# Optimization experiments

Measured on AMD Instinct MI355X. Metric: run time of the kernel, lower is better.

Reference implementation:

```python
import jax, jax.numpy as jnp
import numpy as np

B, C, H, W = 8, 256, 64, 64


def setup_inputs() -> dict:
    key = jax.random.key(0)
    ks = jax.random.split(key, 8)
    s = 1.0 / np.sqrt(C)
    return {
        "x": jax.random.normal(ks[0], (B, C, H, W), dtype=jnp.float32),
        "Wq": jax.random.normal(ks[1], (C, C), dtype=jnp.float32) * s,
        "bq": jax.random.normal(ks[2], (C,), dtype=jnp.float32) * 0.01,
        "Wk": jax.random.normal(ks[3], (C, C), dtype=jnp.float32) * s,
        "bk": jax.random.normal(ks[4], (C,), dtype=jnp.float32) * 0.01,
        "Wv": jax.random.normal(ks[5], (C, C), dtype=jnp.float32) * s,
        "bv": jax.random.normal(ks[6], (C,), dtype=jnp.float32) * 0.01,
        "gamma": jax.random.normal(ks[7], (1,), dtype=jnp.float32) * 0.1,
    }


def reference(x, Wq, bq, Wk, bk, Wv, bv, gamma):
    b, c, h, w = x.shape
    xf = x.reshape(b, c, h * w)                       # (B, C, N)
    # 1x1 conv == per-pixel linear: out_c = W @ in_c + bias
    q = jnp.einsum('oc,bcn->bon', Wq, xf) + bq[None, :, None]
    k = jnp.einsum('oc,bcn->bon', Wk, xf) + bk[None, :, None]
    v = jnp.einsum('oc,bcn->bon', Wv, xf) + bv[None, :, None]
    # attention_map[b, i, j] = sum_c q[b, c, i] * k[b, c, j]  (no scaling in original)
    scores = jnp.einsum('bci,bcj->bij', q, k)         # (B, N, N)
    attn = jax.nn.softmax(scores, axis=-1)
    # out[b, c, i] = sum_j v[b, c, j] * attn[b, i, j]
    out = jnp.einsum('bcj,bij->bci', v, attn)
    out = out.reshape(b, c, h, w)
    return x + gamma[0] * out
```

## Files before the change

kernel.cpp:

```cpp
#include <hip/hip_runtime.h>

#define BATCH 8
#define CCH 256
#define NPOS 4096

typedef __bf16 bf16x8 __attribute__((ext_vector_type(8)));
typedef float f32x4 __attribute__((ext_vector_type(4)));
typedef int i32x4 __attribute__((ext_vector_type(4)));

typedef const __attribute__((address_space(1))) void GAS;
typedef __attribute__((address_space(3))) void LAS;

#define CFENCE() __asm__ volatile("" ::: "memory")
#define WAIT_VM8()  do { CFENCE(); __builtin_amdgcn_s_waitcnt(0x0F78); CFENCE(); } while (0)
#define WAIT_LGKM0() do { CFENCE(); __builtin_amdgcn_s_waitcnt(0xC07F); CFENCE(); } while (0)
#define BAR_RAW() do { CFENCE(); __builtin_amdgcn_s_barrier(); CFENCE(); } while (0)

__device__ __forceinline__ unsigned short f2bf(float f) {
  unsigned u = __builtin_bit_cast(unsigned, f);
  u += 0x7fffu + ((u >> 16) & 1u);
  return (unsigned short)(u >> 16);
}

__device__ __forceinline__ bf16x8 ld_bf8(const unsigned short* p) {
  i32x4 t = *reinterpret_cast<const i32x4*>(p);
  return __builtin_bit_cast(bf16x8, t);
}

__global__ void cvt_kernel(const float* __restrict__ Wq,
                           const float* __restrict__ Wk,
                           const float* __restrict__ Wv,
                           unsigned short* __restrict__ dst)
{
  const int idx = blockIdx.x * 256 + threadIdx.x;
  const float* src = (idx < 65536) ? Wq : ((idx < 131072) ? Wk : Wv);
  dst[idx] = f2bf(src[idx & 65535]);
}

__global__ __launch_bounds__(256, 3)
void qkv_kernel(const float* __restrict__ x,
                const unsigned short* __restrict__ Wall,
                const float* __restrict__ bq,
                const float* __restrict__ bk,
                const float* __restrict__ bv,
                unsigned short* __restrict__ qT,
                unsigned short* __restrict__ kT,
                unsigned short* __restrict__ vG)
{
  __shared__ __align__(16) unsigned short xT[64 * 264];
  __shared__ __align__(16) unsigned short tbuf[64 * 72];

  const int b     = blockIdx.x;
  const int i0    = blockIdx.y * 64;
  const int obase = blockIdx.z * 64;
  const int tid = threadIdx.x;
  const int w   = tid >> 6;
  const int l   = tid & 63;
  const int n   = l & 15;
  const int q4  = l >> 4;

  {
    const float* xp = x + ((size_t)b * CCH + tid) * NPOS + i0;
#pragma unroll
    for (int it = 0; it < 16; ++it) {
      f32x4 f = *reinterpret_cast<const f32x4*>(xp + it * 4);
#pragma unroll
      for (int e = 0; e < 4; ++e) xT[(it * 4 + e) * 264 + tid] = f2bf(f[e]);
    }
  }
  __syncthreads();

  const size_t qbase = (size_t)b * NPOS * CCH;

  for (int s = 0; s < 3; ++s) {
    const unsigned short* Wp = Wall + s * 65536 + (size_t)(obase + w * 16 + n) * CCH + q4 * 8;
    bf16x8 wfr[8];
#pragma unroll
    for (int kk = 0; kk < 8; ++kk) wfr[kk] = ld_bf8(Wp + kk * 32);

    const float* bias = (s == 0) ? bq : (s == 1) ? bk : bv;
    float bo[4];
#pragma unroll
    for (int r = 0; r < 4; ++r) bo[r] = bias[obase + w * 16 + q4 * 4 + r];

    f32x4 acc[4];
#pragma unroll
    for (int pt = 0; pt < 4; ++pt) {
      acc[pt] = {0.f, 0.f, 0.f, 0.f};
#pragma unroll
      for (int kk = 0; kk < 8; ++kk) {
        bf16x8 bfr = ld_bf8(&xT[(pt * 16 + n) * 264 + kk * 32 + q4 * 8]);
        acc[pt] = __builtin_amdgcn_mfma_f32_16x16x32_bf16(wfr[kk], bfr, acc[pt], 0, 0, 0);
      }
    }

    if (s) __syncthreads();
    if (s < 2) {
#pragma unroll
      for (int pt = 0; pt < 4; ++pt)
#pragma unroll
        for (int r = 0; r < 4; ++r)
          tbuf[(pt * 16 + n) * 72 + w * 16 + q4 * 4 + r] = f2bf(acc[pt][r] + bo[r]);
    } else {
#pragma unroll
      for (int pt = 0; pt < 4; ++pt)
#pragma unroll
        for (int r = 0; r < 4; ++r)
          tbuf[(w * 16 + q4 * 4 + r) * 72 + pt * 16 + n] = f2bf(acc[pt][r] + bo[r]);
    }
    __syncthreads();

    if (s < 2) {
      unsigned short* dst = (s == 0 ? qT : kT) + qbase;
#pragma unroll
      for (int it = 0; it < 2; ++it) {
        const int idx = it * 256 + tid;
        const int pos = idx >> 3, ow = (idx & 7) * 8;
        i32x4 d = *reinterpret_cast<const i32x4*>(&tbuf[pos * 72 + ow]);
        *reinterpret_cast<i32x4*>(&dst[(size_t)(i0 + pos) * CCH + obase + ow]) = d;
      }
    } else {
#pragma unroll
      for (int it = 0; it < 2; ++it) {
        const int idx = it * 256 + tid;
        const int o = idx >> 3, pw = (idx & 7) * 8;
        i32x4 d = *reinterpret_cast<const i32x4*>(&tbuf[o * 72 + pw]);
        *reinterpret_cast<i32x4*>(&vG[qbase + (size_t)(obase + o) * NPOS + i0 + pw]) = d;
      }
    }
  }
}

__global__ __launch_bounds__(256, 2)
void attn_kernel(const unsigned short* __restrict__ qT,
                 const unsigned short* __restrict__ kT,
                 const unsigned short* __restrict__ vG,
                 const float* __restrict__ x,
                 const float* __restrict__ gamma,
                 float* __restrict__ out)
{
  __shared__ __align__(16) unsigned short kbuf[2][64 * 256];
  __shared__ __align__(16) unsigned short pbuf[64 * 72];
  __shared__ float stat_lds[64];

  const int b   = blockIdx.x;
  const int i0  = blockIdx.y * 64;
  const int tid = threadIdx.x;
  const int w   = tid >> 6;
  const int l   = tid & 63;
  const int n   = l & 15;
  const int q4  = l >> 4;
  const int nsw = n & 7;

  const unsigned short* qTb = qT + (size_t)b * NPOS * CCH;
  const unsigned short* kTb = kT + (size_t)b * NPOS * CCH;
  const unsigned short* vb  = vG + (size_t)b * NPOS * CCH;

  bf16x8 afr[8];
  {
    const unsigned short* qrow = qTb + (size_t)(i0 + w * 16 + n) * CCH + q4 * 8;
#pragma unroll
    for (int kk = 0; kk < 8; ++kk)
      afr[kk] = ld_bf8(qrow + kk * 32);
  }

  {
#pragma unroll
    for (int it = 0; it < 8; ++it) {
      const int t = w * 8 + it;
      const int j = 2 * t + (l >> 5);
      const int gp = l & 31;
      const int g  = gp ^ (j & 7);
      const unsigned short* src = kTb + (size_t)j * CCH + g * 8;
      unsigned short* dst = &kbuf[0][t * 512];
      __builtin_amdgcn_global_load_lds((GAS*)src, (LAS*)dst, 16, 0, 0);
    }
  }

  f32x4 O[16];
#pragma unroll
  for (int t = 0; t < 16; ++t) O[t] = {0.f, 0.f, 0.f, 0.f};
  float mrow[4] = {-1e30f, -1e30f, -1e30f, -1e30f};
  float lrow[4] = {0.f, 0.f, 0.f, 0.f};

  for (int jt = 0; jt < 64; ++jt) {
    const int j0 = jt * 64;
    const unsigned short* kb = kbuf[jt & 1];

    i32x4 vreg[8];
#pragma unroll
    for (int ct = 0; ct < 4; ++ct) {
      const unsigned short* vp = vb + (size_t)(w * 64 + ct * 16 + n) * NPOS + j0 + q4 * 8;
      vreg[ct * 2]     = *reinterpret_cast<const i32x4*>(vp);
      vreg[ct * 2 + 1] = *reinterpret_cast<const i32x4*>(vp + 32);
    }

    WAIT_VM8();
    BAR_RAW();

    f32x4 sacc[4];
#pragma unroll
    for (int nt = 0; nt < 4; ++nt) {
      const unsigned short* krow = kb + (nt * 16 + n) * 256;
      sacc[nt] = {0.f, 0.f, 0.f, 0.f};
#pragma unroll
      for (int kk = 0; kk < 8; ++kk) {
        const int gp = (kk * 4 + q4) ^ nsw;
        bf16x8 bfr = ld_bf8(krow + gp * 8);
        sacc[nt] = __builtin_amdgcn_mfma_f32_16x16x32_bf16(afr[kk], bfr, sacc[nt], 0, 0, 0);
      }
    }

    float a_r[4];
#pragma unroll
    for (int r = 0; r < 4; ++r) {
      float tm = fmaxf(fmaxf(sacc[0][r], sacc[1][r]), fmaxf(sacc[2][r], sacc[3][r]));
      tm = fmaxf(tm, __shfl_xor(tm, 1));
      tm = fmaxf(tm, __shfl_xor(tm, 2));
      tm = fmaxf(tm, __shfl_xor(tm, 4));
      tm = fmaxf(tm, __shfl_xor(tm, 8));
      const float mnew = fmaxf(mrow[r], tm);
      a_r[r] = __expf(mrow[r] - mnew);
      float s = 0.f;
#pragma unroll
      for (int nt = 0; nt < 4; ++nt) {
        const float p = __expf(sacc[nt][r] - mnew);
        sacc[nt][r] = p;
        s += p;
      }
      s += __shfl_xor(s, 1);
      s += __shfl_xor(s, 2);
      s += __shfl_xor(s, 4);
      s += __shfl_xor(s, 8);
      lrow[r] = lrow[r] * a_r[r] + s;
      mrow[r] = mnew;
    }

    if (n == 0) {
#pragma unroll
      for (int r = 0; r < 4; ++r) stat_lds[w * 16 + q4 * 4 + r] = a_r[r];
    }
#pragma unroll
    for (int r = 0; r < 4; ++r) {
      const int row = w * 16 + q4 * 4 + r;
#pragma unroll
      for (int nt = 0; nt < 4; ++nt)
        pbuf[row * 72 + nt * 16 + n] = f2bf(sacc[nt][r]);
    }

    {
      const int j0n = ((jt + 1) & 63) * 64;
      unsigned short* bufn = kbuf[(jt + 1) & 1];
#pragma unroll
      for (int it = 0; it < 8; ++it) {
        const int t = w * 8 + it;
        const int j = 2 * t + (l >> 5);
        const int gp = l & 31;
        const int g  = gp ^ (j & 7);
        const unsigned short* src = kTb + (size_t)(j0n + j) * CCH + g * 8;
        unsigned short* dst = &bufn[t * 512];
        __builtin_amdgcn_global_load_lds((GAS*)src, (LAS*)dst, 16, 0, 0);
      }
    }

    WAIT_LGKM0();
    BAR_RAW();

#pragma unroll
    for (int it = 0; it < 4; ++it) {
      const float al = stat_lds[it * 16 + n];
#pragma unroll
      for (int ct = 0; ct < 4; ++ct) {
        f32x4& o = O[ct * 4 + it];
        o[0] *= al; o[1] *= al; o[2] *= al; o[3] *= al;
      }
    }

    bf16x8 pf[8];
#pragma unroll
    for (int it = 0; it < 4; ++it) {
      pf[it * 2 + 0] = ld_bf8(&pbuf[(it * 16 + n) * 72 + q4 * 8]);
      pf[it * 2 + 1] = ld_bf8(&pbuf[(it * 16 + n) * 72 + 32 + q4 * 8]);
    }
#pragma unroll
    for (int ct = 0; ct < 4; ++ct) {
      bf16x8 vf0 = __builtin_bit_cast(bf16x8, vreg[ct * 2]);
      bf16x8 vf1 = __builtin_bit_cast(bf16x8, vreg[ct * 2 + 1]);
#pragma unroll
      for (int it = 0; it < 4; ++it) {
        O[ct * 4 + it] = __builtin_amdgcn_mfma_f32_16x16x32_bf16(vf0, pf[it * 2 + 0], O[ct * 4 + it], 0, 0, 0);
        O[ct * 4 + it] = __builtin_amdgcn_mfma_f32_16x16x32_bf16(vf1, pf[it * 2 + 1], O[ct * 4 + it], 0, 0, 0);
      }
    }
  }

  __syncthreads();
  if (n == 0) {
#pragma unroll
    for (int r = 0; r < 4; ++r) stat_lds[w * 16 + q4 * 4 + r] = lrow[r];
  }
  __syncthreads();

  const float g = gamma[0];
#pragma unroll
  for (int it = 0; it < 4; ++it) {
    const float sc = g / stat_lds[it * 16 + n];
    const int ipos = i0 + it * 16 + n;
#pragma unroll
    for (int ct = 0; ct < 4; ++ct) {
#pragma unroll
      for (int r = 0; r < 4; ++r) {
        const int c = w * 64 + ct * 16 + q4 * 4 + r;
        const size_t idx = ((size_t)(b * CCH + c)) * NPOS + ipos;
        out[idx] = x[idx] + sc * O[ct * 4 + it][r];
      }
    }
  }
}

extern "C" void kernel_launch(void* const* d_in, const int* in_sizes, int n_in,
                              void* d_out, int out_size, void* d_ws, size_t ws_size,
                              hipStream_t stream)
{
  const float* x     = (const float*)d_in[0];
  const float* Wq    = (const float*)d_in[1];
  const float* bq    = (const float*)d_in[2];
  const float* Wk    = (const float*)d_in[3];
  const float* bk    = (const float*)d_in[4];
  const float* Wv    = (const float*)d_in[5];
  const float* bv    = (const float*)d_in[6];
  const float* gamma = (const float*)d_in[7];
  float* out = (float*)d_out;

  unsigned short* ws   = (unsigned short*)d_ws;
  unsigned short* Wall = ws;
  unsigned short* qT   = ws + 196608;
  unsigned short* kT   = qT + (size_t)BATCH * NPOS * CCH;
  unsigned short* vG   = kT + (size_t)BATCH * NPOS * CCH;

  cvt_kernel<<<768, 256, 0, stream>>>(Wq, Wk, Wv, Wall);
  qkv_kernel<<<dim3(8, 64, 4), 256, 0, stream>>>(x, Wall, bq, bk, bv, qT, kT, vG);
  attn_kernel<<<dim3(8, 64), 256, 0, stream>>>(qT, kT, vG, x, gamma, out);
}
```

Before: 352.0 us.

## Fold log2e into Q, use exp2 and DPP reductions, swizzle P buffer, merge QKV channel blocks

The Q projection is pre-scaled by log2(e) so the softmax can use a native exp2 instead of __expf. Row max and sum reductions switch from shfl_xor to DPP row_ror operations. The P tile in LDS drops its padding and uses an XOR swizzle to avoid bank conflicts. The QKV kernel now loops over all four output-channel blocks per workgroup, so x is loaded and converted once instead of four times, at the cost of a quarter as many blocks and more serial work per block. DPP row_ror gives a rotation rather than an xor butterfly, but after four steps each lane still holds the full 16-lane reduction.

New measurement: 314.4 us. -10.7%, faster.

```diff
diff --git a/kernel.cpp b/kernel.cpp
--- a/kernel.cpp
+++ b/kernel.cpp
@@ -3,6 +3,7 @@
 #define BATCH 8
 #define CCH 256
 #define NPOS 4096
+#define LOG2E 1.4426950408889634f
 
 typedef __bf16 bf16x8 __attribute__((ext_vector_type(8)));
 typedef float f32x4 __attribute__((ext_vector_type(4)));
@@ -25,6 +26,20 @@
 __device__ __forceinline__ bf16x8 ld_bf8(const unsigned short* p) {
   i32x4 t = *reinterpret_cast<const i32x4*>(p);
   return __builtin_bit_cast(bf16x8, t);
+}
+
+template<int CTRL>
+__device__ __forceinline__ float dpp_rorf(float x) {
+  return __builtin_bit_cast(float,
+      __builtin_amdgcn_update_dpp(0, __builtin_bit_cast(int, x), CTRL, 0xF, 0xF, false));
+}
+
+__device__ __forceinline__ float fexp2(float x) {
+#if __has_builtin(__builtin_amdgcn_exp2f)
+  return __builtin_amdgcn_exp2f(x);
+#else
+  return __expf(x * 0.6931471805599453f);
+#endif
 }
 
 __global__ void cvt_kernel(const float* __restrict__ Wq,
@@ -50,9 +65,8 @@
   __shared__ __align__(16) unsigned short xT[64 * 264];
   __shared__ __align__(16) unsigned short tbuf[64 * 72];
 
-  const int b     = blockIdx.x;
-  const int i0    = blockIdx.y * 64;
-  const int obase = blockIdx.z * 64;
+  const int b   = blockIdx.x;
+  const int i0  = blockIdx.y * 64;
   const int tid = threadIdx.x;
   const int w   = tid >> 6;
   const int l   = tid & 63;
@@ -60,72 +74,81 @@
   const int q4  = l >> 4;
 
   {
-    const float* xp = x + ((size_t)b * CCH + tid) * NPOS + i0;
+    const int li = tid & 15;
+    const int cg = tid >> 4;
 #pragma unroll
     for (int it = 0; it < 16; ++it) {
-      f32x4 f = *reinterpret_cast<const f32x4*>(xp + it * 4);
-#pragma unroll
-      for (int e = 0; e < 4; ++e) xT[(it * 4 + e) * 264 + tid] = f2bf(f[e]);
+      const int c = it * 16 + cg;
+      f32x4 f = *reinterpret_cast<const f32x4*>(x + ((size_t)b * CCH + c) * NPOS + i0 + li * 4);
+#pragma unroll
+      for (int e = 0; e < 4; ++e) xT[(li * 4 + e) * 264 + c] = f2bf(f[e]);
     }
   }
   __syncthreads();
 
   const size_t qbase = (size_t)b * NPOS * CCH;
+  bool first = true;
 
   for (int s = 0; s < 3; ++s) {
-    const unsigned short* Wp = Wall + s * 65536 + (size_t)(obase + w * 16 + n) * CCH + q4 * 8;
-    bf16x8 wfr[8];
-#pragma unroll
-    for (int kk = 0; kk < 8; ++kk) wfr[kk] = ld_bf8(Wp + kk * 32);
-
     const float* bias = (s == 0) ? bq : (s == 1) ? bk : bv;
-    float bo[4];
-#pragma unroll
-    for (int r = 0; r < 4; ++r) bo[r] = bias[obase + w * 16 + q4 * 4 + r];
-
-    f32x4 acc[4];
-#pragma unroll
-    for (int pt = 0; pt < 4; ++pt) {
-      acc[pt] = {0.f, 0.f, 0.f, 0.f};
-#pragma unroll
-      for (int kk = 0; kk < 8; ++kk) {
-        bf16x8 bfr = ld_bf8(&xT[(pt * 16 + n) * 264 + kk * 32 + q4 * 8]);
-        acc[pt] = __builtin_amdgcn_mfma_f32_16x16x32_bf16(wfr[kk], bfr, acc[pt], 0, 0, 0);
-      }
-    }
-
-    if (s) __syncthreads();
-    if (s < 2) {
-#pragma unroll
-      for (int pt = 0; pt < 4; ++pt)
-#pragma unroll
-        for (int r = 0; r < 4; ++r)
-          tbuf[(pt * 16 + n) * 72 + w * 16 + q4 * 4 + r] = f2bf(acc[pt][r] + bo[r]);
-    } else {
-#pragma unroll
-      for (int pt = 0; pt < 4; ++pt)
-#pragma unroll
-        for (int r = 0; r < 4; ++r)
-          tbuf[(w * 16 + q4 * 4 + r) * 72 + pt * 16 + n] = f2bf(acc[pt][r] + bo[r]);
-    }
-    __syncthreads();
-
-    if (s < 2) {
-      unsigned short* dst = (s == 0 ? qT : kT) + qbase;
-#pragma unroll
-      for (int it = 0; it < 2; ++it) {
-        const int idx = it * 256 + tid;
-        const int pos = idx >> 3, ow = (idx & 7) * 8;
-        i32x4 d = *reinterpret_cast<const i32x4*>(&tbuf[pos * 72 + ow]);
-        *reinterpret_cast<i32x4*>(&dst[(size_t)(i0 + pos) * CCH + obase + ow]) = d;
-      }
-    } else {
-#pragma unroll
-      for (int it = 0; it < 2; ++it) {
-        const int idx = it * 256 + tid;
-        const int o = idx >> 3, pw = (idx & 7) * 8;
-        i32x4 d = *reinterpret_cast<const i32x4*>(&tbuf[o * 72 + pw]);
-        *reinterpret_cast<i32x4*>(&vG[qbase + (size_t)(obase + o) * NPOS + i0 + pw]) = d;
+    for (int op = 0; op < 4; ++op) {
+      const int obase = op * 64;
+
+      const unsigned short* Wp = Wall + s * 65536 + (size_t)(obase + w * 16 + n) * CCH + q4 * 8;
+      bf16x8 wfr[8];
+#pragma unroll
+      for (int kk = 0; kk < 8; ++kk) wfr[kk] = ld_bf8(Wp + kk * 32);
+
+      float bo[4];
+#pragma unroll
+      for (int r = 0; r < 4; ++r) bo[r] = bias[obase + w * 16 + q4 * 4 + r];
+
+      f32x4 acc[4];
+#pragma unroll
+      for (int pt = 0; pt < 4; ++pt) {
+        acc[pt] = {0.f, 0.f, 0.f, 0.f};
+#pragma unroll
+        for (int kk = 0; kk < 8; ++kk) {
+          bf16x8 bfr = ld_bf8(&xT[(pt * 16 + n) * 264 + kk * 32 + q4 * 8]);
+          acc[pt] = __builtin_amdgcn_mfma_f32_16x16x32_bf16(wfr[kk], bfr, acc[pt], 0, 0, 0);
+        }
+      }
+
+      if (!first) __syncthreads();
+      first = false;
+      if (s < 2) {
+        const float sc = (s == 0) ? LOG2E : 1.0f;
+#pragma unroll
+        for (int pt = 0; pt < 4; ++pt)
+#pragma unroll
+          for (int r = 0; r < 4; ++r)
+            tbuf[(pt * 16 + n) * 72 + w * 16 + q4 * 4 + r] = f2bf((acc[pt][r] + bo[r]) * sc);
+      } else {
+#pragma unroll
+        for (int pt = 0; pt < 4; ++pt)
+#pragma unroll
+          for (int r = 0; r < 4; ++r)
+            tbuf[(w * 16 + q4 * 4 + r) * 72 + pt * 16 + n] = f2bf(acc[pt][r] + bo[r]);
+      }
+      __syncthreads();
+
+      if (s < 2) {
+        unsigned short* dst = (s == 0 ? qT : kT) + qbase;
+#pragma unroll
+        for (int it2 = 0; it2 < 2; ++it2) {
+          const int idx = it2 * 256 + tid;
+          const int pos = idx >> 3, ow = (idx & 7) * 8;
+          i32x4 d = *reinterpret_cast<const i32x4*>(&tbuf[pos * 72 + ow]);
+          *reinterpret_cast<i32x4*>(&dst[(size_t)(i0 + pos) * CCH + obase + ow]) = d;
+        }
+      } else {
+#pragma unroll
+        for (int it2 = 0; it2 < 2; ++it2) {
+          const int idx = it2 * 256 + tid;
+          const int o = idx >> 3, pw = (idx & 7) * 8;
+          i32x4 d = *reinterpret_cast<const i32x4*>(&tbuf[o * 72 + pw]);
+          *reinterpret_cast<i32x4*>(&vG[qbase + (size_t)(obase + o) * NPOS + i0 + pw]) = d;
+        }
       }
     }
   }
@@ -140,7 +163,7 @@
                  float* __restrict__ out)
 {
   __shared__ __align__(16) unsigned short kbuf[2][64 * 256];
-  __shared__ __align__(16) unsigned short pbuf[64 * 72];
+  __shared__ __align__(16) unsigned short pbuf[64 * 64];
   __shared__ float stat_lds[64];
 
   const int b   = blockIdx.x;
@@ -215,23 +238,23 @@
 #pragma unroll
     for (int r = 0; r < 4; ++r) {
       float tm = fmaxf(fmaxf(sacc[0][r], sacc[1][r]), fmaxf(sacc[2][r], sacc[3][r]));
-      tm = fmaxf(tm, __shfl_xor(tm, 1));
-      tm = fmaxf(tm, __shfl_xor(tm, 2));
-      tm = fmaxf(tm, __shfl_xor(tm, 4));
-      tm = fmaxf(tm, __shfl_xor(tm, 8));
+      tm = fmaxf(tm, dpp_rorf<0x121>(tm));
+      tm = fmaxf(tm, dpp_rorf<0x122>(tm));
+      tm = fmaxf(tm, dpp_rorf<0x124>(tm));
+      tm = fmaxf(tm, dpp_rorf<0x128>(tm));
       const float mnew = fmaxf(mrow[r], tm);
-      a_r[r] = __expf(mrow[r] - mnew);
+      a_r[r] = fexp2(mrow[r] - mnew);
       float s = 0.f;
 #pragma unroll
       for (int nt = 0; nt < 4; ++nt) {
-        const float p = __expf(sacc[nt][r] - mnew);
+        const float p = fexp2(sacc[nt][r] - mnew);
         sacc[nt][r] = p;
         s += p;
       }
-      s += __shfl_xor(s, 1);
-      s += __shfl_xor(s, 2);
-      s += __shfl_xor(s, 4);
-      s += __shfl_xor(s, 8);
+      s += dpp_rorf<0x121>(s);
+      s += dpp_rorf<0x122>(s);
+      s += dpp_rorf<0x124>(s);
+      s += dpp_rorf<0x128>(s);
       lrow[r] = lrow[r] * a_r[r] + s;
       mrow[r] = mnew;
     }
@@ -243,9 +266,12 @@
 #pragma unroll
     for (int r = 0; r < 4; ++r) {
       const int row = w * 16 + q4 * 4 + r;
-#pragma unroll
-      for (int nt = 0; nt < 4; ++nt)
-        pbuf[row * 72 + nt * 16 + n] = f2bf(sacc[nt][r]);
+      const int rs  = row & 7;
+#pragma unroll
+      for (int nt = 0; nt < 4; ++nt) {
+        const int g = nt * 2 + (n >> 3);
+        pbuf[row * 64 + ((g ^ rs) << 3) + (n & 7)] = f2bf(sacc[nt][r]);
+      }
     }
 
     {
@@ -279,8 +305,9 @@
     bf16x8 pf[8];
 #pragma unroll
     for (int it = 0; it < 4; ++it) {
-      pf[it * 2 + 0] = ld_bf8(&pbuf[(it * 16 + n) * 72 + q4 * 8]);
-      pf[it * 2 + 1] = ld_bf8(&pbuf[(it * 16 + n) * 72 + 32 + q4 * 8]);
+      const int rowb = (it * 16 + n) * 64;
+      pf[it * 2 + 0] = ld_bf8(&pbuf[rowb + ((q4 ^ nsw) << 3)]);
+      pf[it * 2 + 1] = ld_bf8(&pbuf[rowb + (((4 + q4) ^ nsw) << 3)]);
     }
 #pragma unroll
     for (int ct = 0; ct < 4; ++ct) {
@@ -339,6 +366,6 @@
   unsigned short* vG   = kT + (size_t)BATCH * NPOS * CCH;
 
   cvt_kernel<<<768, 256, 0, stream>>>(Wq, Wk, Wv, Wall);
-  qkv_kernel<<<dim3(8, 64, 4), 256, 0, stream>>>(x, Wall, bq, bk, bv, qT, kT, vG);
+  qkv_kernel<<<dim3(8, 64), 256, 0, stream>>>(x, Wall, bq, bk, bv, qT, kT, vG);
   attn_kernel<<<dim3(8, 64), 256, 0, stream>>>(qT, kT, vG, x, gamma, out);
 }
```
